# Kernel tuning notes

Hardware: AMD Instinct MI355X
Metric: run time of the kernel (lower is better)

Reference implementation:

```python
import jax, jax.numpy as jnp
import numpy as np

B, V = 16, 262144

def _make_T():
    # 16x9 spherical-harmonics -> 4x4 irradiance transform matrix (Ramamoorthi & Hanrahan)
    c = np.array([0.429043, 0.511664, 0.743125, 0.886227, 0.247708])
    rows = np.array(list(range(16)) + [15])
    cols = np.array([8, 4, 7, 3, 4, 8, 5, 1, 7, 5, 6, 2, 3, 1, 2, 0, 6])
    vals = np.array([c[0], c[0], c[0], c[1],
                     c[0], -c[0], c[0], c[1],
                     c[0], c[0], c[2], c[1],
                     c[1], c[1], c[1], c[3], -c[4]])
    T = np.zeros((16, 9), dtype=np.float32)
    T[rows, cols] = vals  # no duplicate (row, col) pairs
    return jnp.asarray(T)


def setup_inputs() -> dict:
    key = jax.random.key(0)
    k1, k2, k3 = jax.random.split(key, 3)
    light = jax.random.normal(k1, (3,), dtype=jnp.float32)
    normals = jax.random.normal(k2, (B, V, 3), dtype=jnp.float32)
    sh_coeffs = jax.random.normal(k3, (27,), dtype=jnp.float32)  # 9 SH coeffs per RGB channel
    return {"light": light, "normals": normals, "sh_coeffs": sh_coeffs}


def reference(light, normals, sh_coeffs):
    b, v = normals.shape[0], normals.shape[1]
    # augment normals with homogeneous 1 -> [B, V, 4]
    N = jnp.concatenate([normals, jnp.ones((b, v, 1), dtype=normals.dtype)], axis=2)
    T = _make_T()
    # per-channel 4x4 transform: M[c] = (T @ sh9_c).reshape(4, 4)
    M = (T @ sh_coeffs.reshape(3, 9).T).T.reshape(3, 4, 4)  # [3, 4, 4]
    # MN[c, b] = M[c] @ N[b].T  -> [3, B, 4, V]
    MN = jnp.einsum('cij,bvj->cbiv', M, N)
    # faithful to torch: MN[c,b] (shape [4,V]) is row-major .view()'d to [V,4]
    MNr = MN.reshape(3, b, v, 4)
    # per-vertex dot product, stacked over RGB -> [B, V, 3]
    E_rgb = jnp.einsum('bvj,cbvj->bvc', N, MNr)
    return E_rgb
```

## Files before the change

### kernel.cpp

```cpp
#include <hip/hip_runtime.h>


#define SH_V 262144
#define SH_B 16

__global__ __launch_bounds__(256, 8) void sh_lighting_kernel(
    const float* __restrict__ normals,
    const float* __restrict__ sh,
    float* __restrict__ out)
{
    __shared__ float nbr[256 * 12];

    const int tid  = threadIdx.x;
    const int lane = tid & 63;
    const int w    = tid >> 6;
    const int blk  = blockIdx.x;
    const int b    = blk >> 10;
    const int rem  = blk & 1023;
    const int v0   = rem << 8;
    const int i    = rem >> 8;
    const int nb0  = (rem & 255) << 10;

    const float* nbase = normals + (size_t)b * (SH_V * 3);

    {
        const float* src = nbase + (size_t)nb0 * 3;
#pragma unroll
        for (int k = 0; k < 3; ++k) {
            const int idx = 192 * w + 64 * k + lane;
            __builtin_amdgcn_global_load_lds(
                (const __attribute__((address_space(1))) void*)(src + (size_t)idx * 4),
                (__attribute__((address_space(3))) void*)(&nbr[idx * 4]),
                16, 0, 0);
        }
    }

    const float3 own = *(const float3*)(nbase + (size_t)(v0 + tid) * 3);

    const float c0 = 0.429043f, c1 = 0.511664f, c2 = 0.743125f,
                c3 = 0.886227f, c4 = 0.247708f;
    float Mr[3][4];
#pragma unroll
    for (int c = 0; c < 3; ++c) {
        const float L0 = sh[9*c+0], L1 = sh[9*c+1], L2 = sh[9*c+2];
        const float L3 = sh[9*c+3], L4 = sh[9*c+4], L5 = sh[9*c+5];
        const float L6 = sh[9*c+6], L7 = sh[9*c+7], L8 = sh[9*c+8];
        if (i == 0) {
            Mr[c][0] = c0*L8;  Mr[c][1] = c0*L4;  Mr[c][2] = c0*L7;  Mr[c][3] = c1*L3;
        } else if (i == 1) {
            Mr[c][0] = c0*L4;  Mr[c][1] = -c0*L8; Mr[c][2] = c0*L5;  Mr[c][3] = c1*L1;
        } else if (i == 2) {
            Mr[c][0] = c0*L7;  Mr[c][1] = c0*L5;  Mr[c][2] = c2*L6;  Mr[c][3] = c1*L2;
        } else {
            Mr[c][0] = c1*L3;  Mr[c][1] = c1*L1;  Mr[c][2] = c1*L2;  Mr[c][3] = c3*L0 - c4*L6;
        }
    }

    asm volatile("s_waitcnt vmcnt(0)" ::: "memory");
    __builtin_amdgcn_sched_barrier(0);

    const float4* lp = (const float4*)(&nbr[12 * tid]);
    const float4 q0 = lp[0], q1 = lp[1], q2 = lp[2];
    const float ng[12] = {q0.x,q0.y,q0.z,q0.w, q1.x,q1.y,q1.z,q1.w, q2.x,q2.y,q2.z,q2.w};

    const float dx = fmaf(own.x, ng[0], fmaf(own.y, ng[3], fmaf(own.z, ng[6], ng[9])));
    const float dy = fmaf(own.x, ng[1], fmaf(own.y, ng[4], fmaf(own.z, ng[7], ng[10])));
    const float dz = fmaf(own.x, ng[2], fmaf(own.y, ng[5], fmaf(own.z, ng[8], ng[11])));
    const float dw = own.x + own.y + own.z + 1.0f;

    float3 ev;
    ev.x = fmaf(Mr[0][0], dx, fmaf(Mr[0][1], dy, fmaf(Mr[0][2], dz, Mr[0][3] * dw)));
    ev.y = fmaf(Mr[1][0], dx, fmaf(Mr[1][1], dy, fmaf(Mr[1][2], dz, Mr[1][3] * dw)));
    ev.z = fmaf(Mr[2][0], dx, fmaf(Mr[2][1], dy, fmaf(Mr[2][2], dz, Mr[2][3] * dw)));

    *(float3*)(out + (size_t)b * (SH_V * 3) + (size_t)(v0 + tid) * 3) = ev;
}

extern "C" void kernel_launch(void* const* d_in, const int* in_sizes, int n_in,
                              void* d_out, int out_size, void* d_ws, size_t ws_size,
                              hipStream_t stream) {
    const float* normals = (const float*)d_in[1];
    const float* sh      = (const float*)d_in[2];
    float* out           = (float*)d_out;

    const int grid = SH_B * (SH_V / 256);
    sh_lighting_kernel<<<grid, 256, 0, stream>>>(normals, sh, out);
}
```

Measured before the change: 26.62 us.

## Reuse each LDS normal tile across four output quarters per block

Each block now handles the same 256-position slot in all four quarters of the vertex range. The 12-float group it stages in LDS is loaded once and reused for all four rows of M, which cuts the redundant LDS staging loads fourfold and shrinks the grid to a quarter. Output writes become scalar nontemporal stores, which may fragment the previously vectorized float3 store. Each thread also holds more registers and issues four strided own-normal loads, and fewer blocks means less parallelism to hide latency.

```diff
diff --git a/kernel.cpp b/kernel.cpp
--- a/kernel.cpp
+++ b/kernel.cpp
@@ -3,23 +3,23 @@
 
 #define SH_V 262144
 #define SH_B 16
+#define QTR  65536
 
 __global__ __launch_bounds__(256, 8) void sh_lighting_kernel(
     const float* __restrict__ normals,
     const float* __restrict__ sh,
     float* __restrict__ out)
 {
-    __shared__ float nbr[256 * 12];
+    __shared__ float nbr[3072];
 
     const int tid  = threadIdx.x;
     const int lane = tid & 63;
     const int w    = tid >> 6;
     const int blk  = blockIdx.x;
-    const int b    = blk >> 10;
-    const int rem  = blk & 1023;
-    const int v0   = rem << 8;
-    const int i    = rem >> 8;
-    const int nb0  = (rem & 255) << 10;
+    const int b    = blk >> 8;
+    const int ublk = blk & 255;
+    const int u0   = ublk << 8;
+    const int nb0  = u0 << 2;
 
     const float* nbase = normals + (size_t)b * (SH_V * 3);
 
@@ -35,25 +35,24 @@
         }
     }
 
-    const float3 own = *(const float3*)(nbase + (size_t)(v0 + tid) * 3);
+    float3 own[4];
+#pragma unroll
+    for (int m = 0; m < 4; ++m) {
+        own[m] = *(const float3*)(nbase + (size_t)(u0 + tid + m * QTR) * 3);
+    }
 
     const float c0 = 0.429043f, c1 = 0.511664f, c2 = 0.743125f,
                 c3 = 0.886227f, c4 = 0.247708f;
-    float Mr[3][4];
+    float M[3][4][4];
 #pragma unroll
     for (int c = 0; c < 3; ++c) {
         const float L0 = sh[9*c+0], L1 = sh[9*c+1], L2 = sh[9*c+2];
         const float L3 = sh[9*c+3], L4 = sh[9*c+4], L5 = sh[9*c+5];
         const float L6 = sh[9*c+6], L7 = sh[9*c+7], L8 = sh[9*c+8];
-        if (i == 0) {
-            Mr[c][0] = c0*L8;  Mr[c][1] = c0*L4;  Mr[c][2] = c0*L7;  Mr[c][3] = c1*L3;
-        } else if (i == 1) {
-            Mr[c][0] = c0*L4;  Mr[c][1] = -c0*L8; Mr[c][2] = c0*L5;  Mr[c][3] = c1*L1;
-        } else if (i == 2) {
-            Mr[c][0] = c0*L7;  Mr[c][1] = c0*L5;  Mr[c][2] = c2*L6;  Mr[c][3] = c1*L2;
-        } else {
-            Mr[c][0] = c1*L3;  Mr[c][1] = c1*L1;  Mr[c][2] = c1*L2;  Mr[c][3] = c3*L0 - c4*L6;
-        }
+        M[c][0][0] = c0*L8;  M[c][0][1] = c0*L4;  M[c][0][2] = c0*L7;  M[c][0][3] = c1*L3;
+        M[c][1][0] = c0*L4;  M[c][1][1] = -c0*L8; M[c][1][2] = c0*L5;  M[c][1][3] = c1*L1;
+        M[c][2][0] = c0*L7;  M[c][2][1] = c0*L5;  M[c][2][2] = c2*L6;  M[c][2][3] = c1*L2;
+        M[c][3][0] = c1*L3;  M[c][3][1] = c1*L1;  M[c][3][2] = c1*L2;  M[c][3][3] = c3*L0 - c4*L6;
     }
 
     asm volatile("s_waitcnt vmcnt(0)" ::: "memory");
@@ -63,17 +62,24 @@
     const float4 q0 = lp[0], q1 = lp[1], q2 = lp[2];
     const float ng[12] = {q0.x,q0.y,q0.z,q0.w, q1.x,q1.y,q1.z,q1.w, q2.x,q2.y,q2.z,q2.w};
 
-    const float dx = fmaf(own.x, ng[0], fmaf(own.y, ng[3], fmaf(own.z, ng[6], ng[9])));
-    const float dy = fmaf(own.x, ng[1], fmaf(own.y, ng[4], fmaf(own.z, ng[7], ng[10])));
-    const float dz = fmaf(own.x, ng[2], fmaf(own.y, ng[5], fmaf(own.z, ng[8], ng[11])));
-    const float dw = own.x + own.y + own.z + 1.0f;
+    float* obase = out + (size_t)b * (SH_V * 3);
 
-    float3 ev;
-    ev.x = fmaf(Mr[0][0], dx, fmaf(Mr[0][1], dy, fmaf(Mr[0][2], dz, Mr[0][3] * dw)));
-    ev.y = fmaf(Mr[1][0], dx, fmaf(Mr[1][1], dy, fmaf(Mr[1][2], dz, Mr[1][3] * dw)));
-    ev.z = fmaf(Mr[2][0], dx, fmaf(Mr[2][1], dy, fmaf(Mr[2][2], dz, Mr[2][3] * dw)));
+#pragma unroll
+    for (int m = 0; m < 4; ++m) {
+        const float nx = own[m].x, ny = own[m].y, nz = own[m].z;
+        const float dx = fmaf(nx, ng[0], fmaf(ny, ng[3], fmaf(nz, ng[6], ng[9])));
+        const float dy = fmaf(nx, ng[1], fmaf(ny, ng[4], fmaf(nz, ng[7], ng[10])));
+        const float dz = fmaf(nx, ng[2], fmaf(ny, ng[5], fmaf(nz, ng[8], ng[11])));
+        const float dw = nx + ny + nz + 1.0f;
 
-    *(float3*)(out + (size_t)b * (SH_V * 3) + (size_t)(v0 + tid) * 3) = ev;
+        float* op = obase + (size_t)(u0 + tid + m * QTR) * 3;
+        __builtin_nontemporal_store(
+            fmaf(M[0][m][0], dx, fmaf(M[0][m][1], dy, fmaf(M[0][m][2], dz, M[0][m][3] * dw))), op);
+        __builtin_nontemporal_store(
+            fmaf(M[1][m][0], dx, fmaf(M[1][m][1], dy, fmaf(M[1][m][2], dz, M[1][m][3] * dw))), op + 1);
+        __builtin_nontemporal_store(
+            fmaf(M[2][m][0], dx, fmaf(M[2][m][1], dy, fmaf(M[2][m][2], dz, M[2][m][3] * dw))), op + 2);
+    }
 }
 
 extern "C" void kernel_launch(void* const* d_in, const int* in_sizes, int n_in,
@@ -83,6 +89,6 @@
     const float* sh      = (const float*)d_in[2];
     float* out           = (float*)d_out;
 
-    const int grid = SH_B * (SH_V / 256);
+    const int grid = SH_B * (QTR / 256);
     sh_lighting_kernel<<<grid, 256, 0, stream>>>(normals, sh, out);
 }
```

After: 26.33 us. About the same (-1.1%).
